# Kernel tuning notes

Hardware: AMD Instinct MI355X
Metric: run time of the kernel (lower is better)

Reference implementation:

```python
import jax, jax.numpy as jnp
import numpy as np

N, C, E, H = 50000, 128, 1_600_000, 32
JITTER = 1e-20


def _lin(k, fan_in, fan_out):
    return jax.random.normal(k, (fan_in, fan_out), jnp.float32) / np.sqrt(fan_in)


def setup_inputs() -> dict:
    key = jax.random.key(0)
    ks = jax.random.split(key, 20)
    x = jax.random.normal(ks[0], (N, C), jnp.float32)
    edge_index = jax.random.randint(ks[1], (2, E), 0, N, dtype=jnp.int64)
    inp = {"x": x, "edge_index": edge_index}
    # actor params
    inp["aW"] = _lin(ks[2], C, C); inp["ab"] = jnp.zeros((C,), jnp.float32)
    inp["a1W"] = _lin(ks[3], C, H); inp["a1b"] = jnp.zeros((H,), jnp.float32)
    inp["a2W"] = _lin(ks[4], H, H); inp["a2b"] = jnp.zeros((H,), jnp.float32)
    inp["a3W"] = _lin(ks[5], H, 2); inp["a3b"] = jnp.zeros((2,), jnp.float32)
    # critic params
    inp["cW"] = _lin(ks[6], C, C); inp["cb"] = jnp.zeros((C,), jnp.float32)
    inp["c1W"] = _lin(ks[7], C, H); inp["c1b"] = jnp.zeros((H,), jnp.float32)
    inp["c2W"] = _lin(ks[8], H, H); inp["c2b"] = jnp.zeros((H,), jnp.float32)
    inp["c3W"] = _lin(ks[9], H, 2); inp["c3b"] = jnp.zeros((2,), jnp.float32)
    return inp


def gcn_conv(x, src, dst, W, b):
    """Standard PyG GCNConv: add self-loops, symmetric degree norm, X@W, scatter-add, +bias."""
    n = x.shape[0]
    loop = jnp.arange(n)
    s = jnp.concatenate([src, loop])  # [E+N]
    d = jnp.concatenate([dst, loop])
    deg = jax.ops.segment_sum(jnp.ones_like(d, jnp.float32), d, num_segments=n)
    dinv = jnp.where(deg > 0, jax.lax.rsqrt(deg), 0.0)
    norm = dinv[s] * dinv[d]                     # [E+N]
    h = x @ W                                    # [N, C]
    agg = jax.ops.segment_sum(h[s] * norm[:, None], d, num_segments=n)
    return agg + b


def reference(x, edge_index, aW, ab, a1W, a1b, a2W, a2b, a3W, a3b,
              cW, cb, c1W, c1b, c2W, c2b, c3W, c3b):
    src, dst = edge_index[0], edge_index[1]
    # actor
    h = jax.nn.relu(gcn_conv(x, src, dst, aW, ab)) + x
    h = jax.nn.relu(h @ a1W + a1b)
    h = jax.nn.relu(h @ a2W + a2b)
    a = h @ a3W + a3b                            # [N, 2]
    concentration = jax.nn.softplus(a[:, 0]) + JITTER
    p = jax.nn.softplus(a[:, 1])
    action2_probs = p / jnp.sum(p)
    # critic
    hc = jax.nn.relu(gcn_conv(x, src, dst, cW, cb)) + x
    hc = jnp.sum(hc, axis=0)                     # [C]
    hc = jax.nn.relu(hc @ c1W + c1b)
    hc = jax.nn.relu(hc @ c2W + c2b)
    value = hc @ c3W + c3b                       # [2]
    return (concentration, value, action2_probs)
```

## Files before the change

kernel.cpp:

```cpp
#include <hip/hip_runtime.h>
#include <hip/hip_bf16.h>
#include <hip/hip_fp16.h>
#include <math.h>

#define C 128
#define BCAP 12288

using half8x = __attribute__((ext_vector_type(8))) _Float16;
using half4x = __attribute__((ext_vector_type(4))) _Float16;
using f32x4  = __attribute__((ext_vector_type(4))) float;

__device__ inline float4 h4_to_f4(uint2 u) {
    __half2 p0 = *(__half2*)&u.x;
    __half2 p1 = *(__half2*)&u.y;
    float2 f0 = __half22float2(p0), f1 = __half22float2(p1);
    return make_float4(f0.x, f0.y, f1.x, f1.y);
}

__device__ inline float softplusf(float v) {
    return (v > 20.f) ? v : log1pf(expf(v));
}

__global__ __launch_bounds__(256) void initk(unsigned* gcur, float* colsum, float* pSum) {
    int t = threadIdx.x;
    gcur[t] = 0u;
    if (t < 128) colsum[t] = 0.f;
    if (t == 128) pSum[0] = 0.f;
}

__global__ __launch_bounds__(256) void wtk(const float* __restrict__ aW, const float* __restrict__ cW,
                                           const float* __restrict__ a1W,
                                           __half* __restrict__ wt, __half* __restrict__ a1wt) {
    int idx = blockIdx.x * 256 + threadIdx.x;
    if (idx < 32768) {
        int y = idx >> 14, r = idx & 16383;
        int k = r >> 7, n = r & 127;
        const float* W = y ? cW : aW;
        wt[((size_t)y << 14) + n * 128 + k] = __float2half(W[k * 128 + n]);
    } else if (idx < 36864) {
        int r = idx - 32768;
        int k = r >> 5, n = r & 31;
        a1wt[n * 128 + k] = __float2half(a1W[k * 32 + n]);
    }
}

__global__ __launch_bounds__(256) void bink(const int* __restrict__ ei,
                                            unsigned* __restrict__ gcur,
                                            unsigned* __restrict__ gstage,
                                            int E, int NBKT) {
    __shared__ unsigned raw[6400];
    __shared__ unsigned image[6400];
    __shared__ unsigned cnt[256];
    __shared__ unsigned pref[256];
    __shared__ unsigned cur[256];
    __shared__ unsigned gb[256];
    int t = threadIdx.x, b = blockIdx.x;
    int elo = (int)((long long)b * E / 256);
    int ehi = (int)((long long)(b + 1) * E / 256);
    int n = ehi - elo;

    for (int i = t; i < n; i += 256) {
        int d = __builtin_nontemporal_load(ei + E + elo + i);
        int s = __builtin_nontemporal_load(ei + elo + i);
        raw[i] = (unsigned)s | ((unsigned)(d & 255) << 16) | ((unsigned)(d >> 8) << 24);
    }
    cnt[t] = 0u; cur[t] = 0u;
    __syncthreads();
    for (int i = t; i < n; i += 256) atomicAdd(&cnt[raw[i] >> 24], 1u);
    __syncthreads();
    pref[t] = cnt[t];
    __syncthreads();
    for (int off = 1; off < 256; off <<= 1) {
        unsigned add = (t >= off) ? pref[t - off] : 0u;
        __syncthreads();
        pref[t] += add;
        __syncthreads();
    }
    gb[t] = (t < NBKT && cnt[t]) ? atomicAdd(&gcur[t], cnt[t]) : 0u;
    __syncthreads();
    for (int i = t; i < n; i += 256) {
        unsigned v = raw[i];
        unsigned B = v >> 24;
        unsigned pos = (pref[B] - cnt[B]) + atomicAdd(&cur[B], 1u);
        image[pos] = v & 0xFFFFFFu;
    }
    __syncthreads();
    int wv = t >> 6, lane = t & 63;
    for (int B = wv; B < NBKT; B += 4) {
        unsigned c = cnt[B];
        if (!c) continue;
        unsigned eb = pref[B] - c;
        unsigned gbase = gb[B];
        unsigned c2 = (gbase < BCAP) ? ((c < BCAP - gbase) ? c : BCAP - gbase) : 0u;
        for (unsigned i = lane; i < c2; i += 64)
            gstage[(size_t)B * BCAP + gbase + i] = image[eb + i];
    }
}

__global__ void bktscank(const unsigned* __restrict__ gcur, unsigned* __restrict__ bktbase, int NBKT) {
    __shared__ unsigned tmp[256];
    int t = threadIdx.x;
    unsigned g = (t < NBKT) ? gcur[t] : 0u;
    unsigned v = (g < BCAP) ? g : BCAP;
    tmp[t] = v;
    __syncthreads();
    for (int off = 1; off < 256; off <<= 1) {
        unsigned add = (t >= off) ? tmp[t - off] : 0u;
        __syncthreads();
        tmp[t] += add;
        __syncthreads();
    }
    if (t < NBKT) bktbase[t] = tmp[t] - v;
}

__global__ __launch_bounds__(256) void placek(const unsigned* __restrict__ gstage,
                                              const unsigned* __restrict__ gcur,
                                              const unsigned* __restrict__ bktbase,
                                              int* __restrict__ rowptr, float* __restrict__ dinv,
                                              int* __restrict__ col, int N, int NBKT) {
    __shared__ unsigned image[BCAP];
    __shared__ unsigned cnt[256];
    __shared__ unsigned pref[256];
    __shared__ unsigned cur[256];
    int B = blockIdx.x, t = threadIdx.x;
    unsigned g = gcur[B];
    unsigned m = (g < BCAP) ? g : BCAP;
    unsigned base = bktbase[B];
    const unsigned* st = gstage + (size_t)B * BCAP;

    cnt[t] = 0u; cur[t] = 0u;
    __syncthreads();
    for (unsigned i = t; i < m; i += 256) atomicAdd(&cnt[(st[i] >> 16) & 255u], 1u);
    __syncthreads();
    pref[t] = cnt[t];
    __syncthreads();
    for (int off = 1; off < 256; off <<= 1) {
        unsigned add = (t >= off) ? pref[t - off] : 0u;
        __syncthreads();
        pref[t] += add;
        __syncthreads();
    }
    int d = B * 256 + t;
    if (d < N) {
        rowptr[d] = (int)(base + pref[t] - cnt[t]);
        dinv[d] = rsqrtf((float)(cnt[t] + 1u));
    }
    if (B == NBKT - 1 && t == 0) rowptr[N] = (int)(base + m);
    for (unsigned i = t; i < m; i += 256) {
        unsigned v = st[i];
        unsigned dl = (v >> 16) & 255u;
        unsigned pos = (pref[dl] - cnt[dl]) + atomicAdd(&cur[dl], 1u);
        image[pos] = v & 0xFFFFu;
    }
    __syncthreads();
    for (unsigned i = t; i < m; i += 256) col[base + i] = (int)image[i];
}

__global__ __launch_bounds__(256) void xhk(const float* __restrict__ x, const float* __restrict__ dinv,
                                           __half* __restrict__ xh, __half* __restrict__ x16, int N) {
    int i = blockIdx.x * 256 + threadIdx.x;
    if (i >= N * 64) return;
    int node = i >> 6, fp = (i & 63) * 2;
    float w = dinv[node];
    float2 f = *(const float2*)&x[(size_t)node * C + fp];
    __half2 h = __floats2half2_rn(f.x * w, f.y * w);
    __half2 hx = __floats2half2_rn(f.x, f.y);
    *(unsigned*)&xh[(size_t)node * C + fp] = *(unsigned*)&h;
    *(unsigned*)&x16[(size_t)node * C + fp] = *(unsigned*)&hx;
}

__global__ __launch_bounds__(256) void gatherk(const int* __restrict__ col,
                                               const int* __restrict__ rowptr,
                                               const __half* __restrict__ xh,
                                               const float* __restrict__ dinv,
                                               __half* __restrict__ gg, int N) {
    __shared__ int snb[4][64];
    int t = threadIdx.x;
    int wid = t >> 6, lane = t & 63;
    int d = blockIdx.x * 4 + wid;
    if (d >= N) return;
    int beg = rowptr[d], end = rowptr[d + 1];
    int half = lane >> 5, sub = lane & 31;
    int f = sub * 4;

    float a0 = 0.f, a1 = 0.f, a2 = 0.f, a3 = 0.f;

    for (int c = beg; c < end; c += 64) {
        if (c + lane < end) snb[wid][lane] = col[c + lane];
        int n = end - c; if (n > 64) n = 64;
        int j = 0;
        for (; j + 3 < n; j += 4) {
            size_t i0 = (size_t)snb[wid][j + half] * C + f;
            size_t i1 = (size_t)snb[wid][j + 2 + half] * C + f;
            float4 v0 = h4_to_f4(*(const uint2*)&xh[i0]);
            float4 v1 = h4_to_f4(*(const uint2*)&xh[i1]);
            a0 += v0.x + v1.x;
            a1 += v0.y + v1.y;
            a2 += v0.z + v1.z;
            a3 += v0.w + v1.w;
        }
        for (; j < n; j += 2) {
            if (j + half < n) {
                float4 v = h4_to_f4(*(const uint2*)&xh[(size_t)snb[wid][j + half] * C + f]);
                a0 += v.x; a1 += v.y; a2 += v.z; a3 += v.w;
            }
        }
    }
    a0 += __shfl_xor(a0, 32, 64);
    a1 += __shfl_xor(a1, 32, 64);
    a2 += __shfl_xor(a2, 32, 64);
    a3 += __shfl_xor(a3, 32, 64);

    if (half == 0) {
        float4 s4 = h4_to_f4(*(const uint2*)&xh[(size_t)d * C + f]);
        float dv = dinv[d];
        __half2 h0 = __floats2half2_rn((a0 + s4.x) * dv, (a1 + s4.y) * dv);
        __half2 h1 = __floats2half2_rn((a2 + s4.z) * dv, (a3 + s4.w) * dv);
        uint2 u; u.x = *(unsigned*)&h0; u.y = *(unsigned*)&h1;
        *(uint2*)&gg[(size_t)d * C + f] = u;
    }
}

__global__ __launch_bounds__(256) void gemm2k(const __half* __restrict__ gg,
                                              const __half* __restrict__ wt,
                                              const __half* __restrict__ a1wt,
                                              const float* __restrict__ ab, const float* __restrict__ cb,
                                              const __half* __restrict__ x16,
                                              const float* __restrict__ a1b,
                                              const float* __restrict__ a2W, const float* __restrict__ a2b,
                                              const float* __restrict__ a3W, const float* __restrict__ a3b,
                                              float* __restrict__ scratch,
                                              float* __restrict__ out, float* __restrict__ pSum, int N) {
    __shared__ char As[16384];
    __shared__ char Act[16384];
    __shared__ char Aux[8448];
    _Float16* w2t = (_Float16*)Aux;
    _Float16* h1b = (_Float16*)(Aux + 2560);
    float* w3s    = (float*)(Aux + 7680);
    float* scol   = (float*)(Aux + 7936);

    const int row0 = blockIdx.x * 64;
    const int t = threadIdx.x;

#pragma unroll
    for (int i = 0; i < 4; ++i) {
        int c = t + i * 256;
        int row = c >> 4, cb16 = (c & 15) * 16;
        int grow = row0 + row;
        uint4 u = make_uint4(0u, 0u, 0u, 0u);
        if (grow < N) u = *(const uint4*)&gg[(size_t)grow * C + (c & 15) * 8];
        *(uint4*)(As + row * 256 + (cb16 ^ ((row & 7) << 4))) = u;
    }
#pragma unroll
    for (int i = 0; i < 4; ++i) {
        int idx = t + i * 256;
        int k = idx >> 5, n = idx & 31;
        w2t[n * 40 + k] = (_Float16)a2W[idx];
    }
    if (t < 64) w3s[t] = a3W[t];
    __syncthreads();

    int wv = t >> 6, l = t & 63;
    int lm = l & 15, lk = l >> 4;
    int koffB = lk * 16;
    int koffH = lk * 8;

    const __half* WA = wt;
    const __half* WC = wt + 16384;

#pragma unroll
    for (int nc2 = 0; nc2 < 2; ++nc2) {
        const int nc = wv * 2 + nc2;
        const __half* wpA = WA + (nc * 16 + lm) * 128;
        const __half* wpC = WC + (nc * 16 + lm) * 128;
        half8x bfA[4], bfC[4];
#pragma unroll
        for (int kc = 0; kc < 4; ++kc) {
            bfA[kc] = *(const half8x*)(wpA + kc * 32 + koffH);
            bfC[kc] = *(const half8x*)(wpC + kc * 32 + koffH);
        }
        float4 bvA = *(const float4*)&ab[nc * 16 + lk * 4];
        float4 bvC = *(const float4*)&cb[nc * 16 + lk * 4];
        float v0 = 0.f, v1 = 0.f, v2 = 0.f, v3 = 0.f;

#pragma unroll
        for (int rg = 0; rg < 4; ++rg) {
            int rowA = rg * 16 + lm;
            int grow = row0 + rowA;
            bool valid = grow < N;
            int sw = (rowA & 7) << 4;
            const char* rp = As + rowA * 256;
            f32x4 accA = {0.f, 0.f, 0.f, 0.f};
            f32x4 accC = {0.f, 0.f, 0.f, 0.f};
#pragma unroll
            for (int kc = 0; kc < 4; ++kc) {
                half8x afr = *(const half8x*)(rp + ((kc * 64 + koffB) ^ sw));
                accA = __builtin_amdgcn_mfma_f32_16x16x32_f16(bfA[kc], afr, accA, 0, 0, 0);
                accC = __builtin_amdgcn_mfma_f32_16x16x32_f16(bfC[kc], afr, accC, 0, 0, 0);
            }
            half4x xq = {};
            if (valid) xq = *(const half4x*)&x16[(size_t)grow * C + nc * 16 + lk * 4];
            half4x hv = { (_Float16)(valid ? fmaxf(accA[0] + bvA.x, 0.f) + (float)xq[0] : 0.f),
                          (_Float16)(valid ? fmaxf(accA[1] + bvA.y, 0.f) + (float)xq[1] : 0.f),
                          (_Float16)(valid ? fmaxf(accA[2] + bvA.z, 0.f) + (float)xq[2] : 0.f),
                          (_Float16)(valid ? fmaxf(accA[3] + bvA.w, 0.f) + (float)xq[3] : 0.f) };
            *(half4x*)(Act + rowA * 256 + ((nc * 32 + lk * 8) ^ sw)) = hv;
            v0 += valid ? fmaxf(accC[0] + bvC.x, 0.f) + (float)xq[0] : 0.f;
            v1 += valid ? fmaxf(accC[1] + bvC.y, 0.f) + (float)xq[1] : 0.f;
            v2 += valid ? fmaxf(accC[2] + bvC.z, 0.f) + (float)xq[2] : 0.f;
            v3 += valid ? fmaxf(accC[3] + bvC.w, 0.f) + (float)xq[3] : 0.f;
        }
        v0 += __shfl_xor(v0, 1, 64); v0 += __shfl_xor(v0, 2, 64);
        v0 += __shfl_xor(v0, 4, 64); v0 += __shfl_xor(v0, 8, 64);
        v1 += __shfl_xor(v1, 1, 64); v1 += __shfl_xor(v1, 2, 64);
        v1 += __shfl_xor(v1, 4, 64); v1 += __shfl_xor(v1, 8, 64);
        v2 += __shfl_xor(v2, 1, 64); v2 += __shfl_xor(v2, 2, 64);
        v2 += __shfl_xor(v2, 4, 64); v2 += __shfl_xor(v2, 8, 64);
        v3 += __shfl_xor(v3, 1, 64); v3 += __shfl_xor(v3, 2, 64);
        v3 += __shfl_xor(v3, 4, 64); v3 += __shfl_xor(v3, 8, 64);
        if (lm == 0)
            *(float4*)&scol[nc * 16 + lk * 4] = make_float4(v0, v1, v2, v3);
    }
    __syncthreads();

    if (t < 128)
        scratch[(size_t)blockIdx.x * 128 + t] = scol[t];

    const int rowM = wv * 16 + lm;
    const int growM = row0 + rowM;
    const bool validM = growM < N;
    const int swM = (rowM & 7) << 4;

    half8x a1f[4];
    {
        const char* rp = Act + rowM * 256;
#pragma unroll
        for (int kc = 0; kc < 4; ++kc)
            a1f[kc] = *(const half8x*)(rp + ((kc * 64 + koffB) ^ swM));
    }
#pragma unroll
    for (int ct = 0; ct < 2; ++ct) {
        const __half* ap = a1wt + (ct * 16 + lm) * 128;
        f32x4 acc1 = {0.f, 0.f, 0.f, 0.f};
#pragma unroll
        for (int kc = 0; kc < 4; ++kc) {
            half8x bq = *(const half8x*)(ap + kc * 32 + koffH);
            acc1 = __builtin_amdgcn_mfma_f32_16x16x32_f16(bq, a1f[kc], acc1, 0, 0, 0);
        }
        float4 b1v = *(const float4*)&a1b[ct * 16 + lk * 4];
        half4x h = { (_Float16)fmaxf(acc1[0] + b1v.x, 0.f),
                     (_Float16)fmaxf(acc1[1] + b1v.y, 0.f),
                     (_Float16)fmaxf(acc1[2] + b1v.z, 0.f),
                     (_Float16)fmaxf(acc1[3] + b1v.w, 0.f) };
        *(half4x*)((char*)h1b + rowM * 80 + ct * 32 + lk * 8) = h;
    }

    half4x alo = *(const half4x*)((char*)h1b + rowM * 80 + lk * 16);
    half4x ahi = *(const half4x*)((char*)h1b + rowM * 80 + lk * 16 + 8);
    half8x a2f = __builtin_shufflevector(alo, ahi, 0, 1, 2, 3, 4, 5, 6, 7);
    float p0 = 0.f, p1 = 0.f;
#pragma unroll
    for (int ct = 0; ct < 2; ++ct) {
        half4x blo = *(const half4x*)((char*)w2t + (ct * 16 + lm) * 80 + lk * 16);
        half4x bhi = *(const half4x*)((char*)w2t + (ct * 16 + lm) * 80 + lk * 16 + 8);
        half8x b2f = __builtin_shufflevector(blo, bhi, 0, 1, 2, 3, 4, 5, 6, 7);
        f32x4 acc2 = {0.f, 0.f, 0.f, 0.f};
        acc2 = __builtin_amdgcn_mfma_f32_16x16x32_f16(b2f, a2f, acc2, 0, 0, 0);
        float4 b2v = *(const float4*)&a2b[ct * 16 + lk * 4];
#pragma unroll
        for (int j = 0; j < 4; ++j) {
            int f = ct * 16 + lk * 4 + j;
            float h2v = fmaxf(acc2[j] + (&b2v.x)[j], 0.f);
            float2 w3 = *(const float2*)&w3s[f * 2];
            p0 += h2v * w3.x;
            p1 += h2v * w3.y;
        }
    }
    p0 += __shfl_xor(p0, 16, 64); p0 += __shfl_xor(p0, 32, 64);
    p1 += __shfl_xor(p1, 16, 64); p1 += __shfl_xor(p1, 32, 64);
    float wave_psum = 0.f;
    if (lk == 0 && validM) {
        float s0 = softplusf(p0 + a3b[0]);
        float s1 = softplusf(p1 + a3b[1]);
        out[growM] = s0 + 1e-20f;
        out[(size_t)N + 2 + growM] = s1;
        wave_psum = s1;
    }
    wave_psum += __shfl_xor(wave_psum, 1, 64);
    wave_psum += __shfl_xor(wave_psum, 2, 64);
    wave_psum += __shfl_xor(wave_psum, 4, 64);
    wave_psum += __shfl_xor(wave_psum, 8, 64);
    wave_psum += __shfl_xor(wave_psum, 16, 64);
    wave_psum += __shfl_xor(wave_psum, 32, 64);
    if (l == 0) atomicAdd(pSum, wave_psum);
}

__global__ __launch_bounds__(128) void csredk(const float* __restrict__ scratch, float* __restrict__ colsum, int nblk) {
    int t = threadIdx.x;
    float s = 0.f;
    for (int b = blockIdx.x; b < nblk; b += gridDim.x)
        s += scratch[(size_t)b * 128 + t];
    atomicAdd(&colsum[t], s);
}

__global__ void critick(const float* __restrict__ colsum,
                        const float* __restrict__ c1W, const float* __restrict__ c1b,
                        const float* __restrict__ c2W, const float* __restrict__ c2b,
                        const float* __restrict__ c3W, const float* __restrict__ c3b,
                        float* __restrict__ out, int N) {
    __shared__ float s1[32], s2[32];
    int t = threadIdx.x;
    if (t < 32) {
        float acc = c1b[t];
        for (int k = 0; k < 128; ++k) acc += colsum[k] * c1W[k * 32 + t];
        s1[t] = fmaxf(acc, 0.f);
    }
    __syncthreads();
    if (t < 32) {
        float acc = c2b[t];
        for (int k = 0; k < 32; ++k) acc += s1[k] * c2W[k * 32 + t];
        s2[t] = fmaxf(acc, 0.f);
    }
    __syncthreads();
    if (t < 2) {
        float acc = c3b[t];
        for (int k = 0; k < 32; ++k) acc += s2[k] * c3W[k * 2 + t];
        out[(size_t)N + t] = acc;
    }
}

__global__ __launch_bounds__(256) void normk(float* __restrict__ out, const float* __restrict__ pSum, int N) {
    int i = blockIdx.x * 256 + threadIdx.x;
    if (i < N) out[(size_t)N + 2 + i] /= pSum[0];
}

extern "C" void kernel_launch(void* const* d_in, const int* in_sizes, int n_in,
                              void* d_out, int out_size, void* d_ws, size_t ws_size,
                              hipStream_t stream) {
    const float* x   = (const float*)d_in[0];
    const int* ei    = (const int*)d_in[1];
    const float* aW  = (const float*)d_in[2];
    const float* ab  = (const float*)d_in[3];
    const float* a1W = (const float*)d_in[4];
    const float* a1b = (const float*)d_in[5];
    const float* a2W = (const float*)d_in[6];
    const float* a2b = (const float*)d_in[7];
    const float* a3W = (const float*)d_in[8];
    const float* a3b = (const float*)d_in[9];
    const float* cW  = (const float*)d_in[10];
    const float* cb  = (const float*)d_in[11];
    const float* c1W = (const float*)d_in[12];
    const float* c1b = (const float*)d_in[13];
    const float* c2W = (const float*)d_in[14];
    const float* c2b = (const float*)d_in[15];
    const float* c3W = (const float*)d_in[16];
    const float* c3b = (const float*)d_in[17];

    const int N = in_sizes[0] / C;
    const int E = in_sizes[1] / 2;
    const int NBKT = (N + 255) / 256;
    const int nblk64 = (N + 63) / 64;
    float* out = (float*)d_out;

    char* ws = (char*)d_ws;
    size_t off = 0;
    auto alloc = [&](size_t bytes) {
        size_t o = off;
        off = (off + bytes + 255) & ~(size_t)255;
        return (void*)(ws + o);
    };
    unsigned* gcur    = (unsigned*)alloc(256 * 4);
    unsigned* bktbase = (unsigned*)alloc(256 * 4);
    unsigned* gstage  = (unsigned*)alloc((size_t)NBKT * BCAP * 4);
    int* rowptr       = (int*)alloc((size_t)(N + 1) * 4);
    float* dinv       = (float*)alloc((size_t)N * 4);
    int* colidx       = (int*)alloc((size_t)E * 4);
    __half* xh        = (__half*)alloc((size_t)N * C * 2);
    __half* x16       = (__half*)alloc((size_t)N * C * 2);
    __half* gg        = (__half*)alloc((size_t)N * C * 2);
    __half* wt        = (__half*)alloc(2 * 16384 * 2);
    __half* a1wt      = (__half*)alloc(4096 * 2);
    float* scratch    = (float*)alloc((size_t)nblk64 * 128 * 4);
    float* colsum     = (float*)alloc(128 * 4);
    float* pSum       = (float*)alloc(4);

    initk<<<1, 256, 0, stream>>>(gcur, colsum, pSum);
    wtk<<<144, 256, 0, stream>>>(aW, cW, a1W, wt, a1wt);
    bink<<<256, 256, 0, stream>>>(ei, gcur, gstage, E, NBKT);
    bktscank<<<1, 256, 0, stream>>>(gcur, bktbase, NBKT);
    placek<<<NBKT, 256, 0, stream>>>(gstage, gcur, bktbase, rowptr, dinv, colidx, N, NBKT);
    xhk<<<(N * 64 + 255) / 256, 256, 0, stream>>>(x, dinv, xh, x16, N);
    gatherk<<<(N + 3) / 4, 256, 0, stream>>>(colidx, rowptr, xh, dinv, gg, N);
    gemm2k<<<nblk64, 256, 0, stream>>>(gg, wt, a1wt, ab, cb, x16,
                                       a1b, a2W, a2b, a3W, a3b,
                                       scratch, out, pSum, N);
    csredk<<<8, 128, 0, stream>>>(scratch, colsum, nblk64);
    critick<<<1, 64, 0, stream>>>(colsum, c1W, c1b, c2W, c2b, c3W, c3b, out, N);
    normk<<<(N + 255) / 256, 256, 0, stream>>>(out, pSum, N);
}
```

Measured before the change: 217.7 us.

## Fold init and bucket-scan kernels into neighbors, prefetch residual, nontemporal col loads

Merges the init kernel into the weight-transpose kernel and recomputes the bucket prefix scan inside each placement block, removing two tiny launches. The GEMM kernel now loads its residual x16 fragments into registers at the start instead of after the MFMAs. Column index loads in the gather use nontemporal hints. This trades redundant per-block scan work and extra register pressure for fewer launches and hidden latency.

```diff
diff --git a/kernel.cpp b/kernel.cpp
--- a/kernel.cpp
+++ b/kernel.cpp
@@ -21,17 +21,17 @@
     return (v > 20.f) ? v : log1pf(expf(v));
 }
 
-__global__ __launch_bounds__(256) void initk(unsigned* gcur, float* colsum, float* pSum) {
-    int t = threadIdx.x;
-    gcur[t] = 0u;
-    if (t < 128) colsum[t] = 0.f;
-    if (t == 128) pSum[0] = 0.f;
-}
-
 __global__ __launch_bounds__(256) void wtk(const float* __restrict__ aW, const float* __restrict__ cW,
                                            const float* __restrict__ a1W,
-                                           __half* __restrict__ wt, __half* __restrict__ a1wt) {
-    int idx = blockIdx.x * 256 + threadIdx.x;
+                                           __half* __restrict__ wt, __half* __restrict__ a1wt,
+                                           unsigned* gcur, float* colsum, float* pSum) {
+    int t = threadIdx.x;
+    if (blockIdx.x == 0) {
+        gcur[t] = 0u;
+        if (t < 128) colsum[t] = 0.f;
+        if (t == 128) pSum[0] = 0.f;
+    }
+    int idx = blockIdx.x * 256 + t;
     if (idx < 32768) {
         int y = idx >> 14, r = idx & 16383;
         int k = r >> 7, n = r & 127;
@@ -97,35 +97,30 @@
     }
 }
 
-__global__ void bktscank(const unsigned* __restrict__ gcur, unsigned* __restrict__ bktbase, int NBKT) {
-    __shared__ unsigned tmp[256];
-    int t = threadIdx.x;
-    unsigned g = (t < NBKT) ? gcur[t] : 0u;
-    unsigned v = (g < BCAP) ? g : BCAP;
-    tmp[t] = v;
-    __syncthreads();
-    for (int off = 1; off < 256; off <<= 1) {
-        unsigned add = (t >= off) ? tmp[t - off] : 0u;
-        __syncthreads();
-        tmp[t] += add;
-        __syncthreads();
-    }
-    if (t < NBKT) bktbase[t] = tmp[t] - v;
-}
-
 __global__ __launch_bounds__(256) void placek(const unsigned* __restrict__ gstage,
                                               const unsigned* __restrict__ gcur,
-                                              const unsigned* __restrict__ bktbase,
                                               int* __restrict__ rowptr, float* __restrict__ dinv,
                                               int* __restrict__ col, int N, int NBKT) {
     __shared__ unsigned image[BCAP];
     __shared__ unsigned cnt[256];
     __shared__ unsigned pref[256];
     __shared__ unsigned cur[256];
+    __shared__ unsigned sbase[256];
     int B = blockIdx.x, t = threadIdx.x;
-    unsigned g = gcur[B];
-    unsigned m = (g < BCAP) ? g : BCAP;
-    unsigned base = bktbase[B];
+
+    unsigned gv = (t < NBKT) ? gcur[t] : 0u;
+    unsigned val = (gv < BCAP) ? gv : BCAP;
+    sbase[t] = val;
+    __syncthreads();
+    for (int off = 1; off < 256; off <<= 1) {
+        unsigned add = (t >= off) ? sbase[t - off] : 0u;
+        __syncthreads();
+        sbase[t] += add;
+        __syncthreads();
+    }
+    unsigned gB = gcur[B];
+    unsigned m = (gB < BCAP) ? gB : BCAP;
+    unsigned base = sbase[B] - m;
     const unsigned* st = gstage + (size_t)B * BCAP;
 
     cnt[t] = 0u; cur[t] = 0u;
@@ -186,7 +181,7 @@
     float a0 = 0.f, a1 = 0.f, a2 = 0.f, a3 = 0.f;
 
     for (int c = beg; c < end; c += 64) {
-        if (c + lane < end) snb[wid][lane] = col[c + lane];
+        if (c + lane < end) snb[wid][lane] = __builtin_nontemporal_load(col + c + lane);
         int n = end - c; if (n > 64) n = 64;
         int j = 0;
         for (; j + 3 < n; j += 4) {
@@ -241,6 +236,22 @@
 
     const int row0 = blockIdx.x * 64;
     const int t = threadIdx.x;
+    const int wv = t >> 6, l = t & 63;
+    const int lm = l & 15, lk = l >> 4;
+    const int koffB = lk * 16;
+    const int koffH = lk * 8;
+
+    uint2 xpre[4][2];
+#pragma unroll
+    for (int rg = 0; rg < 4; ++rg) {
+        int grow = row0 + rg * 16 + lm;
+#pragma unroll
+        for (int nc2 = 0; nc2 < 2; ++nc2) {
+            int nc = wv * 2 + nc2;
+            xpre[rg][nc2] = (grow < N) ? *(const uint2*)&x16[(size_t)grow * C + nc * 16 + lk * 4]
+                                       : make_uint2(0u, 0u);
+        }
+    }
 
 #pragma unroll
     for (int i = 0; i < 4; ++i) {
@@ -259,11 +270,6 @@
     }
     if (t < 64) w3s[t] = a3W[t];
     __syncthreads();
-
-    int wv = t >> 6, l = t & 63;
-    int lm = l & 15, lk = l >> 4;
-    int koffB = lk * 16;
-    int koffH = lk * 8;
 
     const __half* WA = wt;
     const __half* WC = wt + 16384;
@@ -298,8 +304,7 @@
                 accA = __builtin_amdgcn_mfma_f32_16x16x32_f16(bfA[kc], afr, accA, 0, 0, 0);
                 accC = __builtin_amdgcn_mfma_f32_16x16x32_f16(bfC[kc], afr, accC, 0, 0, 0);
             }
-            half4x xq = {};
-            if (valid) xq = *(const half4x*)&x16[(size_t)grow * C + nc * 16 + lk * 4];
+            half4x xq = *(half4x*)&xpre[rg][nc2];
             half4x hv = { (_Float16)(valid ? fmaxf(accA[0] + bvA.x, 0.f) + (float)xq[0] : 0.f),
                           (_Float16)(valid ? fmaxf(accA[1] + bvA.y, 0.f) + (float)xq[1] : 0.f),
                           (_Float16)(valid ? fmaxf(accA[2] + bvA.z, 0.f) + (float)xq[2] : 0.f),
@@ -470,7 +475,6 @@
         return (void*)(ws + o);
     };
     unsigned* gcur    = (unsigned*)alloc(256 * 4);
-    unsigned* bktbase = (unsigned*)alloc(256 * 4);
     unsigned* gstage  = (unsigned*)alloc((size_t)NBKT * BCAP * 4);
     int* rowptr       = (int*)alloc((size_t)(N + 1) * 4);
     float* dinv       = (float*)alloc((size_t)N * 4);
@@ -484,11 +488,9 @@
     float* colsum     = (float*)alloc(128 * 4);
     float* pSum       = (float*)alloc(4);
 
-    initk<<<1, 256, 0, stream>>>(gcur, colsum, pSum);
-    wtk<<<144, 256, 0, stream>>>(aW, cW, a1W, wt, a1wt);
+    wtk<<<144, 256, 0, stream>>>(aW, cW, a1W, wt, a1wt, gcur, colsum, pSum);
     bink<<<256, 256, 0, stream>>>(ei, gcur, gstage, E, NBKT);
-    bktscank<<<1, 256, 0, stream>>>(gcur, bktbase, NBKT);
-    placek<<<NBKT, 256, 0, stream>>>(gstage, gcur, bktbase, rowptr, dinv, colidx, N, NBKT);
+    placek<<<NBKT, 256, 0, stream>>>(gstage, gcur, rowptr, dinv, colidx, N, NBKT);
     xhk<<<(N * 64 + 255) / 256, 256, 0, stream>>>(x, dinv, xh, x16, N);
     gatherk<<<(N + 3) / 4, 256, 0, stream>>>(colidx, rowptr, xh, dinv, gg, N);
     gemm2k<<<nblk64, 256, 0, stream>>>(gg, wt, a1wt, ab, cb, x16,
```

Result: faster. 210.8 us (-3.2%).
